# Kernel optimization log

Measured on AMD Instinct MI355X. Metric: run time of the kernel, lower is better.

Reference implementation:

```python
import jax, jax.numpy as jnp
import numpy as np
import jax.scipy.linalg as jsl

N = 20000
E = 320000
IN_FEAT = 128
HID = 128
OUT_FEAT = 64
D = 4            # stalk_dim
K = HID // D     # number of stalks per node
MLP_HID = 64


def setup_inputs() -> dict:
    key = jax.random.key(0)
    ks = jax.random.split(key, 16)
    def lin(kw, kb, fan_in, fan_out):
        s = 1.0 / np.sqrt(fan_in)
        w = jax.random.uniform(kw, (fan_in, fan_out), minval=-s, maxval=s, dtype=jnp.float32)
        b = jax.random.uniform(kb, (fan_out,), minval=-s, maxval=s, dtype=jnp.float32)
        return w, b
    x = jax.random.normal(ks[0], (N, IN_FEAT), dtype=jnp.float32)
    edge_index = jax.random.randint(ks[1], (2, E), 0, N, dtype=jnp.int64)
    lin_in_w, lin_in_b = lin(ks[2], ks[3], IN_FEAT, HID)
    conv0_w1, conv0_b1 = lin(ks[4], ks[5], 2 * HID, MLP_HID)
    conv0_w2, conv0_b2 = lin(ks[6], ks[7], MLP_HID, 2 * D * D)
    conv1_w1, conv1_b1 = lin(ks[8], ks[9], 2 * HID, MLP_HID)
    conv1_w2, conv1_b2 = lin(ks[10], ks[11], MLP_HID, 2 * D * D)
    lin_out_w, lin_out_b = lin(ks[12], ks[13], HID, OUT_FEAT)
    return {
        "x": x, "edge_index": edge_index,
        "lin_in_w": lin_in_w, "lin_in_b": lin_in_b,
        "conv0_w1": conv0_w1, "conv0_b1": conv0_b1,
        "conv0_w2": conv0_w2, "conv0_b2": conv0_b2, "conv0_eps": jnp.float32(0.5),
        "conv1_w1": conv1_w1, "conv1_b1": conv1_b1,
        "conv1_w2": conv1_w2, "conv1_b2": conv1_b2, "conv1_eps": jnp.float32(0.5),
        "lin_out_w": lin_out_w, "lin_out_b": lin_out_b,
    }


def _sheaf_conv(x, row, col, w1, b1, w2, b2, eps):
    # edge gather -> MLP -> skew-symmetric expm -> batched small matmuls -> scatter-add
    x_row = x[row]              # [E, C] source features
    x_col = x[col]              # [E, C] target features
    h = jax.nn.relu(jnp.concatenate([x_row, x_col], axis=-1) @ w1 + b1)
    maps = (h @ w2 + b2).reshape(-1, 2, D, D)        # [E, 2, d, d]
    A = maps - jnp.swapaxes(maps, -1, -2)            # skew-symmetric
    F_e = jax.vmap(jsl.expm)(A.reshape(-1, D, D)).reshape(-1, 2, D, D)
    f_u, f_v = F_e[:, 0], F_e[:, 1]                  # [E, d, d] each
    # PyG default flow: x_i = x[col] (target), x_j = x[row] (source)
    x_i = x_col.reshape(-1, K, D)
    x_j = x_row.reshape(-1, K, D)
    proj_i = jnp.einsum('eab,ekb->eka', f_u, x_i)
    proj_j = jnp.einsum('eab,ekb->eka', f_v, x_j)
    err = proj_i - proj_j
    msg = jnp.einsum('eba,ekb->eka', f_u, err).reshape(-1, K * D)  # f_u^T @ err
    agg = jax.ops.segment_sum(msg, col, num_segments=x.shape[0])   # scatter-add at target
    return x - eps * agg


def reference(x, edge_index, lin_in_w, lin_in_b,
              conv0_w1, conv0_b1, conv0_w2, conv0_b2, conv0_eps,
              conv1_w1, conv1_b1, conv1_w2, conv1_b2, conv1_eps,
              lin_out_w, lin_out_b):
    row, col = edge_index[0], edge_index[1]
    h = x @ lin_in_w + lin_in_b
    h = jax.nn.elu(_sheaf_conv(h, row, col, conv0_w1, conv0_b1, conv0_w2, conv0_b2, conv0_eps))
    h = jax.nn.elu(_sheaf_conv(h, row, col, conv1_w1, conv1_b1, conv1_w2, conv1_b2, conv1_eps))
    return h @ lin_out_w + lin_out_b
```

## Files before the change

### kernel.cpp

```cpp
#include <hip/hip_runtime.h>
#include <math.h>


using short8 = __attribute__((ext_vector_type(8))) short;
using f32x4 = __attribute__((ext_vector_type(4))) float;
typedef unsigned short u16;

__device__ __forceinline__ u16 f2bf(float f) {
  unsigned u = __float_as_uint(f);
  unsigned r = (u + 0x7FFFu + ((u >> 16) & 1u)) >> 16;
  return (u16)r;
}
__device__ __forceinline__ float bf2f(u16 v) {
  return __uint_as_float(((unsigned)v) << 16);
}

__global__ void __launch_bounds__(256) k_prep(const float* __restrict__ x,
    u16* __restrict__ Xb, int* __restrict__ cnt, int n4, int N,
    const float* __restrict__ win, const float* __restrict__ w1a,
    const float* __restrict__ w1b, const float* __restrict__ wout,
    const float* __restrict__ w2a, const float* __restrict__ w2b,
    const float* __restrict__ b1a, const float* __restrict__ b1b,
    u16* __restrict__ WTin, u16* __restrict__ WT1a, u16* __restrict__ WT1b,
    u16* __restrict__ WTout, u16* __restrict__ W2Ta, u16* __restrict__ W2Tb,
    float* __restrict__ B1pa, float* __restrict__ B1pb) {
  int idx = blockIdx.x * 256 + threadIdx.x;
  if (idx < N) cnt[idx] = 0;
  if (idx < n4) {
    float4 v = ((const float4*)x)[idx];
    ushort4 o;
    o.x = f2bf(v.x);
    o.y = f2bf(v.y);
    o.z = f2bf(v.z);
    o.w = f2bf(v.w);
    ((ushort4*)Xb)[idx] = o;
  }
  if (idx < 16384) {
    int o = idx >> 7, i = idx & 127;
    WTin[idx] = f2bf(win[i * 128 + o]);
  } else if (idx < 32768) {
    int j = idx - 16384;
    int o = j >> 7, i = j & 127;
    WT1a[j] = f2bf(o < 64 ? w1a[i * 64 + o] : w1a[(128 + i) * 64 + (o - 64)]);
  } else if (idx < 49152) {
    int j = idx - 32768;
    int o = j >> 7, i = j & 127;
    WT1b[j] = f2bf(o < 64 ? w1b[i * 64 + o] : w1b[(128 + i) * 64 + (o - 64)]);
  } else if (idx < 57344) {
    int j = idx - 49152;
    int o = j >> 7, i = j & 127;
    WTout[j] = f2bf(wout[i * 64 + o]);
  } else if (idx < 59392) {
    int j = idx - 57344;
    int o = j >> 6, k = j & 63;
    W2Ta[j] = f2bf(w2a[k * 32 + o]);
  } else if (idx < 61440) {
    int j = idx - 59392;
    int o = j >> 6, k = j & 63;
    W2Tb[j] = f2bf(w2b[k * 32 + o]);
  } else if (idx < 61568) {
    int j = idx - 61440;
    B1pa[j] = (j < 64) ? 0.f : b1a[j - 64];
  } else if (idx < 61696) {
    int j = idx - 61568;
    B1pb[j] = (j < 64) ? 0.f : b1b[j - 64];
  }
}

__global__ void __launch_bounds__(256) k_gemm_mfma(const u16* __restrict__ Ab,
    const u16* __restrict__ WT, const float* __restrict__ bias,
    float* __restrict__ C, u16* __restrict__ Cb, int N, int P) {
  int t = threadIdx.x;
  int wv = t >> 6, lane = t & 63;
  int row0 = (blockIdx.x << 6) + (wv << 4);
  int cb = blockIdx.y << 4;
  int col = lane & 15, quad = lane >> 4;
  const u16* wrow = WT + (size_t)(cb + col) * 128 + quad * 8;
  short8 b0 = *(const short8*)(wrow);
  short8 b1 = *(const short8*)(wrow + 32);
  short8 b2 = *(const short8*)(wrow + 64);
  short8 b3 = *(const short8*)(wrow + 96);
  float bv = bias ? bias[cb + col] : 0.f;
  const u16* ar = Ab + (size_t)(row0 + col) * 128 + quad * 8;
  short8 a0 = *(const short8*)(ar);
  short8 a1 = *(const short8*)(ar + 32);
  short8 a2 = *(const short8*)(ar + 64);
  short8 a3 = *(const short8*)(ar + 96);
  f32x4 acc = {0.f, 0.f, 0.f, 0.f};
  acc = __builtin_amdgcn_mfma_f32_16x16x32_bf16(a0, b0, acc, 0, 0, 0);
  acc = __builtin_amdgcn_mfma_f32_16x16x32_bf16(a1, b1, acc, 0, 0, 0);
  acc = __builtin_amdgcn_mfma_f32_16x16x32_bf16(a2, b2, acc, 0, 0, 0);
  acc = __builtin_amdgcn_mfma_f32_16x16x32_bf16(a3, b3, acc, 0, 0, 0);
#pragma unroll
  for (int r = 0; r < 4; ++r) {
    int row = row0 + quad * 4 + r;
    if (row < N) {
      float o = acc[r] + bv;
      if (C) C[(size_t)row * P + cb + col] = o;
      if (Cb) Cb[(size_t)row * 128 + cb + col] = f2bf(o);
    }
  }
}

__global__ void __launch_bounds__(256) k_hist(const int* __restrict__ eidx,
                                              int* __restrict__ cnt, int E) {
  int e = blockIdx.x * 256 + threadIdx.x;
  if (e < E) atomicAdd(&cnt[eidx[E + e]], 1);
}

__global__ void __launch_bounds__(256) k_scanA(const int* __restrict__ cnt,
                                               int* __restrict__ bsum, int N) {
  __shared__ int sums[256];
  int b = blockIdx.x, t = threadIdx.x;
  int base = b * 2048 + t * 8;
  int s = 0;
#pragma unroll
  for (int k = 0; k < 8; ++k) {
    int i = base + k;
    if (i < N) s += cnt[i];
  }
  sums[t] = s;
  __syncthreads();
  for (int d = 128; d > 0; d >>= 1) {
    if (t < d) sums[t] += sums[t + d];
    __syncthreads();
  }
  if (t == 0) bsum[b] = sums[0];
}

__global__ void __launch_bounds__(256) k_scanC(const int* __restrict__ cnt,
    const int* __restrict__ bsum, int* __restrict__ ptr,
    int* __restrict__ cursor, int N, int nblocks) {
  __shared__ int sums[256];
  int b = blockIdx.x, t = threadIdx.x;
  int bo = 0;
  for (int k = 0; k < b; ++k) bo += bsum[k];
  int base = b * 2048 + t * 8;
  int vals[8];
  int s = 0;
#pragma unroll
  for (int k = 0; k < 8; ++k) {
    int i = base + k;
    int c = (i < N) ? cnt[i] : 0;
    vals[k] = s;
    s += c;
  }
  sums[t] = s;
  __syncthreads();
  for (int d = 1; d < 256; d <<= 1) {
    int v = (t >= d) ? sums[t - d] : 0;
    __syncthreads();
    sums[t] += v;
    __syncthreads();
  }
  int toff = (t == 0) ? 0 : sums[t - 1];
#pragma unroll
  for (int k = 0; k < 8; ++k) {
    int i = base + k;
    if (i < N) {
      int p = bo + toff + vals[k];
      ptr[i] = p;
      cursor[i] = p;
    }
  }
  if (b == nblocks - 1 && t == 255) ptr[N] = bo + sums[255];
}

__global__ void __launch_bounds__(256) k_fill(const int* __restrict__ eidx,
    int* __restrict__ cursor, int* __restrict__ adj, int E) {
  int e = blockIdx.x * 256 + threadIdx.x;
  if (e >= E) return;
  int r = eidx[e], c = eidx[E + e];
  int pos = atomicAdd(&cursor[c], 1);
  adj[pos] = r;
}

__device__ __forceinline__ void so4_expm(const float* __restrict__ m,
                                         float* __restrict__ F) {
  float v1 = m[1] - m[4], v2 = m[2] - m[8], v3 = m[3] - m[12];
  float w1 = m[11] - m[14], w2 = m[13] - m[7], w3 = m[6] - m[9];
  float p1 = 0.5f * (v1 + w1), p2 = 0.5f * (v2 + w2), p3 = 0.5f * (v3 + w3);
  float q1 = 0.5f * (v1 - w1), q2 = 0.5f * (v2 - w2), q3 = 0.5f * (v3 - w3);
  float tp2 = p1 * p1 + p2 * p2 + p3 * p3;
  float tq2 = q1 * q1 + q2 * q2 + q3 * q3;
  float tp = sqrtf(tp2), tq = sqrtf(tq2);
  float cp = __cosf(tp);
  float sp = (tp > 1e-6f) ? (__sinf(tp) / tp) : (1.f - tp2 * (1.f / 6.f));
  float cq = __cosf(tq);
  float sq = (tq > 1e-6f) ? (__sinf(tq) / tq) : (1.f - tq2 * (1.f / 6.f));
  float a1 = sp * p1, a2 = sp * p2, a3 = sp * p3;
  float b1 = sq * q1, b2 = sq * q2, b3 = sq * q3;
  float Rp[16] = {cp,  a1,  a2,  a3,  -a1, cp,  a3,  -a2,
                  -a2, -a3, cp,  a1,  -a3, a2,  -a1, cp};
  float Rq[16] = {cq,  b1,  b2,  b3,  -b1, cq,  -b3, b2,
                  -b2, b3,  cq,  -b1, -b3, -b2, b1,  cq};
#pragma unroll
  for (int a = 0; a < 4; ++a)
#pragma unroll
    for (int b = 0; b < 4; ++b) {
      float s = 0.f;
#pragma unroll
      for (int c = 0; c < 4; ++c) s = fmaf(Rp[a * 4 + c], Rq[c * 4 + b], s);
      F[a * 4 + b] = s;
    }
}

__global__ void __launch_bounds__(64) k_conv(const float* __restrict__ x,
    const u16* __restrict__ xgb, const u16* __restrict__ pqb,
    const u16* __restrict__ W2T, const float* __restrict__ b2,
    const int* __restrict__ ptr, const int* __restrict__ adj,
    const float* __restrict__ epsp, float* __restrict__ xout,
    u16* __restrict__ xoutb, int N) {
  __shared__ float ms[16 * 44];
  int lane = threadIdx.x;
  int v = blockIdx.x;
  if (v >= N) return;
  int p0 = ptr[v], p1 = ptr[v + 1];
  int el = lane & 15, quad = lane >> 4;
  int a = lane & 3, kb = lane & ~3;
  short8 bf00 = *(const short8*)(W2T + (size_t)el * 64 + quad * 8);
  short8 bf01 = *(const short8*)(W2T + (size_t)el * 64 + 32 + quad * 8);
  short8 bf10 = *(const short8*)(W2T + (size_t)(16 + el) * 64 + quad * 8);
  short8 bf11 = *(const short8*)(W2T + (size_t)(16 + el) * 64 + 32 + quad * 8);
  float b2a = b2[el], b2b = b2[16 + el];
  short8 qv0 = *(const short8*)(pqb + (size_t)v * 128 + 64 + quad * 8);
  short8 qv1 = *(const short8*)(pqb + (size_t)v * 128 + 96 + quad * 8);
  const float* xv = x + (size_t)v * 128;
  float4 xi1 = *(const float4*)(xv + kb);
  float4 xi2 = *(const float4*)(xv + 64 + kb);
  float hv1 = xv[lane], hv2 = xv[64 + lane];
  float s10 = 0.f, s11 = 0.f, s12 = 0.f, s13 = 0.f;
  float acc1 = 0.f, acc2 = 0.f;
  for (int b0 = p0; b0 < p1; b0 += 16) {
    int nb = p1 - b0;
    nb = (nb > 16) ? 16 : nb;
    int ee = b0 + ((el < nb) ? el : (nb - 1));
    int row = adj[ee];
    f32x4 c0 = {0.f, 0.f, 0.f, 0.f};
    f32x4 c1 = {0.f, 0.f, 0.f, 0.f};
    {
      short8 pv = *(const short8*)(pqb + (size_t)row * 128 + quad * 8);
      union { short8 s; unsigned u[4]; } av;
#pragma unroll
      for (int j2 = 0; j2 < 4; ++j2) {
        float h0 = fmaxf(bf2f((u16)pv[2 * j2]) + bf2f((u16)qv0[2 * j2]), 0.f);
        float h1 = fmaxf(
            bf2f((u16)pv[2 * j2 + 1]) + bf2f((u16)qv0[2 * j2 + 1]), 0.f);
        unsigned r;
        asm("v_cvt_pk_bf16_f32 %0, %1, %2" : "=v"(r) : "v"(h0), "v"(h1));
        av.u[j2] = r;
      }
      c0 = __builtin_amdgcn_mfma_f32_16x16x32_bf16(av.s, bf00, c0, 0, 0, 0);
      c1 = __builtin_amdgcn_mfma_f32_16x16x32_bf16(av.s, bf10, c1, 0, 0, 0);
    }
    {
      short8 pv = *(const short8*)(pqb + (size_t)row * 128 + 32 + quad * 8);
      union { short8 s; unsigned u[4]; } av;
#pragma unroll
      for (int j2 = 0; j2 < 4; ++j2) {
        float h0 = fmaxf(bf2f((u16)pv[2 * j2]) + bf2f((u16)qv1[2 * j2]), 0.f);
        float h1 = fmaxf(
            bf2f((u16)pv[2 * j2 + 1]) + bf2f((u16)qv1[2 * j2 + 1]), 0.f);
        unsigned r;
        asm("v_cvt_pk_bf16_f32 %0, %1, %2" : "=v"(r) : "v"(h0), "v"(h1));
        av.u[j2] = r;
      }
      c0 = __builtin_amdgcn_mfma_f32_16x16x32_bf16(av.s, bf01, c0, 0, 0, 0);
      c1 = __builtin_amdgcn_mfma_f32_16x16x32_bf16(av.s, bf11, c1, 0, 0, 0);
    }
#pragma unroll
    for (int r = 0; r < 4; ++r) {
      ms[(quad * 4 + r) * 44 + el] = c0[r] + b2a;
      ms[(quad * 4 + r) * 44 + 16 + el] = c1[r] + b2b;
    }
    __syncthreads();
    if (lane < 16) {
      float m[32];
      const float* mr = ms + lane * 44;
#pragma unroll
      for (int i = 0; i < 32; ++i) m[i] = mr[i];
      float Fu[16], Fv[16];
      so4_expm(m, Fu);
      so4_expm(m + 16, Fv);
      float* mw = ms + lane * 44;
#pragma unroll
      for (int aa = 0; aa < 4; ++aa)
#pragma unroll
        for (int bb = 0; bb < 4; ++bb) {
          float s1 = 0.f, s2 = 0.f;
#pragma unroll
          for (int cc = 0; cc < 4; ++cc) {
            s1 = fmaf(Fu[cc * 4 + aa], Fu[cc * 4 + bb], s1);
            s2 = fmaf(Fu[cc * 4 + aa], Fv[cc * 4 + bb], s2);
          }
          mw[aa * 4 + bb] = s1;
          mw[16 + aa * 4 + bb] = s2;
        }
    }
    __syncthreads();
    int j = 0;
    for (; j + 1 < nb; j += 2) {
      int r0 = __builtin_amdgcn_readlane(row, j);
      int r1 = __builtin_amdgcn_readlane(row, j + 1);
      float4 am1 = *(const float4*)(ms + j * 44 + a * 4);
      float4 am2 = *(const float4*)(ms + j * 44 + 16 + a * 4);
      float4 bm1 = *(const float4*)(ms + (j + 1) * 44 + a * 4);
      float4 bm2 = *(const float4*)(ms + (j + 1) * 44 + 16 + a * 4);
      ushort4 ya1 = *(const ushort4*)(xgb + (size_t)r0 * 128 + kb);
      ushort4 ya2 = *(const ushort4*)(xgb + (size_t)r0 * 128 + 64 + kb);
      ushort4 yb1 = *(const ushort4*)(xgb + (size_t)r1 * 128 + kb);
      ushort4 yb2 = *(const ushort4*)(xgb + (size_t)r1 * 128 + 64 + kb);
      s10 += am1.x + bm1.x;
      s11 += am1.y + bm1.y;
      s12 += am1.z + bm1.z;
      s13 += am1.w + bm1.w;
      acc1 -= am2.x * bf2f(ya1.x) + am2.y * bf2f(ya1.y) +
              am2.z * bf2f(ya1.z) + am2.w * bf2f(ya1.w);
      acc2 -= am2.x * bf2f(ya2.x) + am2.y * bf2f(ya2.y) +
              am2.z * bf2f(ya2.z) + am2.w * bf2f(ya2.w);
      acc1 -= bm2.x * bf2f(yb1.x) + bm2.y * bf2f(yb1.y) +
              bm2.z * bf2f(yb1.z) + bm2.w * bf2f(yb1.w);
      acc2 -= bm2.x * bf2f(yb2.x) + bm2.y * bf2f(yb2.y) +
              bm2.z * bf2f(yb2.z) + bm2.w * bf2f(yb2.w);
    }
    if (j < nb) {
      int r0 = __builtin_amdgcn_readlane(row, j);
      float4 am1 = *(const float4*)(ms + j * 44 + a * 4);
      float4 am2 = *(const float4*)(ms + j * 44 + 16 + a * 4);
      ushort4 ya1 = *(const ushort4*)(xgb + (size_t)r0 * 128 + kb);
      ushort4 ya2 = *(const ushort4*)(xgb + (size_t)r0 * 128 + 64 + kb);
      s10 += am1.x;
      s11 += am1.y;
      s12 += am1.z;
      s13 += am1.w;
      acc1 -= am2.x * bf2f(ya1.x) + am2.y * bf2f(ya1.y) +
              am2.z * bf2f(ya1.z) + am2.w * bf2f(ya1.w);
      acc2 -= am2.x * bf2f(ya2.x) + am2.y * bf2f(ya2.y) +
              am2.z * bf2f(ya2.z) + am2.w * bf2f(ya2.w);
    }
    __syncthreads();
  }
  acc1 += s10 * xi1.x + s11 * xi1.y + s12 * xi1.z + s13 * xi1.w;
  acc2 += s10 * xi2.x + s11 * xi2.y + s12 * xi2.z + s13 * xi2.w;
  float eps = *epsp;
  float r1 = hv1 - eps * acc1;
  float r2 = hv2 - eps * acc2;
  r1 = (r1 > 0.f) ? r1 : expm1f(r1);
  r2 = (r2 > 0.f) ? r2 : expm1f(r2);
  xout[(size_t)v * 128 + lane] = r1;
  xout[(size_t)v * 128 + 64 + lane] = r2;
  xoutb[(size_t)v * 128 + lane] = f2bf(r1);
  xoutb[(size_t)v * 128 + 64 + lane] = f2bf(r2);
}

extern "C" void kernel_launch(void* const* d_in, const int* in_sizes, int n_in,
                              void* d_out, int out_size, void* d_ws,
                              size_t ws_size, hipStream_t stream) {
  const float* x = (const float*)d_in[0];
  const int* eidx = (const int*)d_in[1];
  const float* lin_in_w = (const float*)d_in[2];
  const float* lin_in_b = (const float*)d_in[3];
  const float* c0w1 = (const float*)d_in[4];
  const float* c0b1 = (const float*)d_in[5];
  const float* c0w2 = (const float*)d_in[6];
  const float* c0b2 = (const float*)d_in[7];
  const float* c0eps = (const float*)d_in[8];
  const float* c1w1 = (const float*)d_in[9];
  const float* c1b1 = (const float*)d_in[10];
  const float* c1w2 = (const float*)d_in[11];
  const float* c1b2 = (const float*)d_in[12];
  const float* c1eps = (const float*)d_in[13];
  const float* lout_w = (const float*)d_in[14];
  const float* lout_b = (const float*)d_in[15];
  float* out = (float*)d_out;

  int N = in_sizes[0] / 128;
  int E = in_sizes[1] / 2;
  int Npad = N + 64;

  char* ws = (char*)d_ws;
  size_t szH = (size_t)N * 128 * 4;
  size_t szHb = (size_t)Npad * 128 * 2;
  float* H = (float*)ws;
  float* H2 = (float*)(ws + szH);
  u16* Xb = (u16*)(ws + 2 * szH);
  u16* Hb = (u16*)(ws + 2 * szH + szHb);
  u16* H2b = (u16*)(ws + 2 * szH + 2 * szHb);
  u16* PQb = (u16*)(ws + 2 * szH + 3 * szHb);
  u16* WTin = (u16*)(ws + 2 * szH + 4 * szHb);
  u16* WT1a = WTin + 16384;
  u16* WT1b = WT1a + 16384;
  u16* WTout = WT1b + 16384;
  u16* W2Ta = WTout + 8192;
  u16* W2Tb = W2Ta + 2048;
  float* B1pa = (float*)(W2Tb + 2048);
  float* B1pb = B1pa + 128;
  char* ip = (char*)(B1pb + 128);
  int* cnt = (int*)ip;
  int* ptr = (int*)(ip + 4 * (size_t)(N + 64));
  int* cursor = (int*)(ip + 8 * (size_t)(N + 64));
  int* adj = (int*)(ip + 12 * (size_t)(N + 64));
  int* bsum = (int*)(ip + 12 * (size_t)(N + 64) + 4 * (size_t)E);

  dim3 blk(256);
  int gN = (N + 63) / 64;
  int gE = (E + 255) / 256;
  int nsb = (N + 2047) / 2048;

  k_prep<<<(N * 32 + 255) / 256, blk, 0, stream>>>(
      x, Xb, cnt, N * 32, N, lin_in_w, c0w1, c1w1, lout_w, c0w2, c1w2, c0b1,
      c1b1, WTin, WT1a, WT1b, WTout, W2Ta, W2Tb, B1pa, B1pb);
  k_hist<<<gE, blk, 0, stream>>>(eidx, cnt, E);
  k_scanA<<<nsb, blk, 0, stream>>>(cnt, bsum, N);
  k_scanC<<<nsb, blk, 0, stream>>>(cnt, bsum, ptr, cursor, N, nsb);
  k_fill<<<gE, blk, 0, stream>>>(eidx, cursor, adj, E);

  k_gemm_mfma<<<dim3(gN, 8), blk, 0, stream>>>(Xb, WTin, lin_in_b, H, Hb, N,
                                               128);

  float* cur = H;
  float* nxt = H2;
  u16* curb = Hb;
  u16* nxtb = H2b;
  for (int layer = 0; layer < 2; ++layer) {
    const u16* wt1 = layer ? WT1b : WT1a;
    const u16* w2t = layer ? W2Tb : W2Ta;
    const float* b1p = layer ? B1pb : B1pa;
    const float* b2 = layer ? c1b2 : c0b2;
    const float* ep = layer ? c1eps : c0eps;
    k_gemm_mfma<<<dim3(gN, 8), blk, 0, stream>>>(curb, wt1, b1p, nullptr, PQb,
                                                 N, 128);
    k_conv<<<N, dim3(64), 0, stream>>>(cur, curb, PQb, w2t, b2, ptr, adj, ep,
                                       nxt, nxtb, N);
    float* tf = cur; cur = nxt; nxt = tf;
    u16* tb = curb; curb = nxtb; nxtb = tb;
  }

  k_gemm_mfma<<<dim3(gN, 4), blk, 0, stream>>>(curb, WTout, lout_b, out,
                                               nullptr, N, 64);
}
```

Baseline: 282.5 us.

## Double-buffer neighbor feature gathers into LDS via async global_load_lds

```diff
diff --git a/kernel.cpp b/kernel.cpp
--- a/kernel.cpp
+++ b/kernel.cpp
@@ -13,6 +13,12 @@
 }
 __device__ __forceinline__ float bf2f(u16 v) {
   return __uint_as_float(((unsigned)v) << 16);
+}
+
+__device__ __forceinline__ void glds16(const void* g, void* l) {
+  __builtin_amdgcn_global_load_lds(
+      (const __attribute__((address_space(1))) unsigned int*)g,
+      (__attribute__((address_space(3))) unsigned int*)l, 16, 0, 0);
 }
 
 __global__ void __launch_bounds__(256) k_prep(const float* __restrict__ x,
@@ -212,12 +218,15 @@
     const float* __restrict__ epsp, float* __restrict__ xout,
     u16* __restrict__ xoutb, int N) {
   __shared__ float ms[16 * 44];
+  __shared__ u16 xs[2][16 * 128];
   int lane = threadIdx.x;
   int v = blockIdx.x;
   if (v >= N) return;
   int p0 = ptr[v], p1 = ptr[v + 1];
   int el = lane & 15, quad = lane >> 4;
   int a = lane & 3, kb = lane & ~3;
+  int sub = lane >> 4;
+  int colb = (lane & 15) * 8;
   short8 bf00 = *(const short8*)(W2T + (size_t)el * 64 + quad * 8);
   short8 bf01 = *(const short8*)(W2T + (size_t)el * 64 + 32 + quad * 8);
   short8 bf10 = *(const short8*)(W2T + (size_t)(16 + el) * 64 + quad * 8);
@@ -231,11 +240,30 @@
   float hv1 = xv[lane], hv2 = xv[64 + lane];
   float s10 = 0.f, s11 = 0.f, s12 = 0.f, s13 = 0.f;
   float acc1 = 0.f, acc2 = 0.f;
+  int cur = 0;
+  int row = 0;
+  if (p0 < p1) {
+    int nb0 = p1 - p0;
+    nb0 = (nb0 > 16) ? 16 : nb0;
+    int ee0 = p0 + ((el < nb0) ? el : (nb0 - 1));
+    row = adj[ee0];
+#pragma unroll
+    for (int t = 0; t < 4; ++t) {
+      int r = __shfl(row, (t << 2) + sub);
+      glds16(xgb + (size_t)r * 128 + colb, &xs[0][t * 512]);
+    }
+  }
   for (int b0 = p0; b0 < p1; b0 += 16) {
     int nb = p1 - b0;
     nb = (nb > 16) ? 16 : nb;
-    int ee = b0 + ((el < nb) ? el : (nb - 1));
-    int row = adj[ee];
+    int have_next = (b0 + 16 < p1);
+    int row_n = row;
+    if (have_next) {
+      int nb2 = p1 - b0 - 16;
+      nb2 = (nb2 > 16) ? 16 : nb2;
+      int ee2 = b0 + 16 + ((el < nb2) ? el : (nb2 - 1));
+      row_n = adj[ee2];
+    }
     f32x4 c0 = {0.f, 0.f, 0.f, 0.f};
     f32x4 c1 = {0.f, 0.f, 0.f, 0.f};
     {
@@ -274,6 +302,13 @@
       ms[(quad * 4 + r) * 44 + 16 + el] = c1[r] + b2b;
     }
     __syncthreads();
+    if (have_next) {
+#pragma unroll
+      for (int t = 0; t < 4; ++t) {
+        int r = __shfl(row_n, (t << 2) + sub);
+        glds16(xgb + (size_t)r * 128 + colb, &xs[cur ^ 1][t * 512]);
+      }
+    }
     if (lane < 16) {
       float m[32];
       const float* mr = ms + lane * 44;
@@ -298,18 +333,23 @@
         }
     }
     __syncthreads();
+    if (have_next) {
+      asm volatile("s_waitcnt vmcnt(4)" ::: "memory");
+    } else {
+      asm volatile("s_waitcnt vmcnt(0)" ::: "memory");
+    }
+    __builtin_amdgcn_sched_barrier(0);
+    const u16* xc = xs[cur];
     int j = 0;
     for (; j + 1 < nb; j += 2) {
-      int r0 = __builtin_amdgcn_readlane(row, j);
-      int r1 = __builtin_amdgcn_readlane(row, j + 1);
       float4 am1 = *(const float4*)(ms + j * 44 + a * 4);
       float4 am2 = *(const float4*)(ms + j * 44 + 16 + a * 4);
       float4 bm1 = *(const float4*)(ms + (j + 1) * 44 + a * 4);
       float4 bm2 = *(const float4*)(ms + (j + 1) * 44 + 16 + a * 4);
-      ushort4 ya1 = *(const ushort4*)(xgb + (size_t)r0 * 128 + kb);
-      ushort4 ya2 = *(const ushort4*)(xgb + (size_t)r0 * 128 + 64 + kb);
-      ushort4 yb1 = *(const ushort4*)(xgb + (size_t)r1 * 128 + kb);
-      ushort4 yb2 = *(const ushort4*)(xgb + (size_t)r1 * 128 + 64 + kb);
+      ushort4 ya1 = *(const ushort4*)(xc + j * 128 + kb);
+      ushort4 ya2 = *(const ushort4*)(xc + j * 128 + 64 + kb);
+      ushort4 yb1 = *(const ushort4*)(xc + (j + 1) * 128 + kb);
+      ushort4 yb2 = *(const ushort4*)(xc + (j + 1) * 128 + 64 + kb);
       s10 += am1.x + bm1.x;
       s11 += am1.y + bm1.y;
       s12 += am1.z + bm1.z;
@@ -324,11 +364,10 @@
               bm2.z * bf2f(yb2.z) + bm2.w * bf2f(yb2.w);
     }
     if (j < nb) {
-      int r0 = __builtin_amdgcn_readlane(row, j);
       float4 am1 = *(const float4*)(ms + j * 44 + a * 4);
       float4 am2 = *(const float4*)(ms + j * 44 + 16 + a * 4);
-      ushort4 ya1 = *(const ushort4*)(xgb + (size_t)r0 * 128 + kb);
-      ushort4 ya2 = *(const ushort4*)(xgb + (size_t)r0 * 128 + 64 + kb);
+      ushort4 ya1 = *(const ushort4*)(xc + j * 128 + kb);
+      ushort4 ya2 = *(const ushort4*)(xc + j * 128 + 64 + kb);
       s10 += am1.x;
       s11 += am1.y;
       s12 += am1.z;
@@ -339,6 +378,8 @@
               am2.z * bf2f(ya2.z) + am2.w * bf2f(ya2.w);
     }
     __syncthreads();
+    row = row_n;
+    cur ^= 1;
   }
   acc1 += s10 * xi1.x + s11 * xi1.y + s12 * xi1.z + s13 * xi1.w;
   acc2 += s10 * xi2.x + s11 * xi2.y + s12 * xi2.z + s13 * xi2.w;
```

Measured after the change: 274.3 us. -2.9%, faster.
